# Performance work log

Hardware: AMD Instinct MI355X
Metric: run time of the kernel (lower is better)

## Reference

```python
import jax, jax.numpy as jnp
import numpy as np

VOCAB = 50257
BATCH = 512
SEQ = 1024


def setup_inputs() -> dict:
    key = jax.random.key(0)
    kx, kidf = jax.random.split(key)
    x = jax.random.randint(kx, (BATCH, SEQ), 0, VOCAB, dtype=jnp.int64)
    # idf weights are positive; uniform in (0.1, 5.0) mimics real idf values
    idf = jax.random.uniform(kidf, (VOCAB,), dtype=jnp.float32, minval=0.1, maxval=5.0)
    return {"x": x, "idf": idf}


def reference(x, idf):
    B, S = x.shape
    V = idf.shape[0]
    # term-frequency histogram: scatter-add directly into (B, V) accumulator,
    # equivalent to the one-hot scatter_ + sum over seq in the original
    rows = jnp.arange(B, dtype=x.dtype)[:, None]           # (B, 1)
    tf = jnp.zeros((B, V), dtype=jnp.float32).at[rows, x].add(1.0)
    tfidf = tf * idf                                        # (B, V)
    n = jnp.sum(tfidf, axis=1, keepdims=True)               # (B, 1)
    return tfidf / n
```

## Files before the change

kernel.cpp:

```cpp
#include <hip/hip_runtime.h>


constexpr int VOCAB   = 50257;
constexpr int SEQ     = 1024;
constexpr int BATCH   = 512;
constexpr int BWORDS  = (VOCAB + 3) / 4;
constexpr int BWORDS4 = ((BWORDS + 3) / 4) * 4;
constexpr int NT      = 1024;
constexpr int NGROUP  = VOCAB >> 2;

struct __attribute__((packed)) f4p { float4 v; };

__global__ __launch_bounds__(NT)
void tfidf_kernel(const int* __restrict__ x,
                  const float* __restrict__ idf,
                  float* __restrict__ out) {
    __shared__ __align__(16) unsigned int cnt[BWORDS4];
    __shared__ float red[NT / 64];

    const int b   = blockIdx.x;
    const int tid = threadIdx.x;

    const int tok = x[(size_t)b * SEQ + tid];

    {
        uint4* z = (uint4*)cnt;
        const uint4 z4 = make_uint4(0u, 0u, 0u, 0u);
        for (int i = tid; i < BWORDS4 / 4; i += NT) z[i] = z4;
    }

    const float my_idf = idf[tok];
    __syncthreads();

    atomicAdd(&cnt[tok >> 2], 1u << ((tok & 3) * 8));

    float v = my_idf;
    #pragma unroll
    for (int off = 32; off > 0; off >>= 1) v += __shfl_down(v, off, 64);
    if ((tid & 63) == 0) red[tid >> 6] = v;
    __syncthreads();
    float nsum = 0.0f;
    #pragma unroll
    for (int w = 0; w < NT / 64; ++w) nsum += red[w];
    const float inv_n = 1.0f / nsum;

    float* __restrict__ orow = out + (size_t)b * VOCAB;
    const float4* __restrict__ idf4 = (const float4*)idf;
    f4p* __restrict__ o4 = (f4p*)orow;

    for (int c = tid; c < NGROUP; c += NT) {
        const unsigned int w = cnt[c];
        const float4 f = idf4[c];
        float4 r;
        r.x = (float)(w & 0xffu)          * f.x * inv_n;
        r.y = (float)((w >> 8)  & 0xffu)  * f.y * inv_n;
        r.z = (float)((w >> 16) & 0xffu)  * f.z * inv_n;
        r.w = (float)(w >> 24)            * f.w * inv_n;
        o4[c].v = r;
    }
    if (tid == 0) {
        orow[VOCAB - 1] =
            (float)(cnt[(VOCAB - 1) >> 2] & 0xffu) * idf[VOCAB - 1] * inv_n;
    }
}

extern "C" void kernel_launch(void* const* d_in, const int* in_sizes, int n_in,
                              void* d_out, int out_size, void* d_ws, size_t ws_size,
                              hipStream_t stream) {
    const int*   x   = (const int*)d_in[0];
    const float* idf = (const float*)d_in[1];
    float*       out = (float*)d_out;
    tfidf_kernel<<<dim3(BATCH), dim3(NT), 0, stream>>>(x, idf, out);
}
```

Measured before the change: 110.8 us.

## Replace shared histogram with zero-fill plus global float atomics per token

Removes the LDS byte-packed histogram and the dense compute pass over the vocabulary. Each row of the output is zero-filled, and after the idf sum is reduced every token atomically adds idf*inv_n into its output slot in global memory. This drops the idf reads and LDS work of the dense pass. In exchange it issues 1024 global float atomics per row, which depend on the zero stores being visible (enforced by a vmcnt wait and a barrier), and float atomic ordering changes rounding slightly.

```diff
diff --git a/kernel.cpp b/kernel.cpp
--- a/kernel.cpp
+++ b/kernel.cpp
@@ -1,13 +1,11 @@
 #include <hip/hip_runtime.h>
 
 
-constexpr int VOCAB   = 50257;
-constexpr int SEQ     = 1024;
-constexpr int BATCH   = 512;
-constexpr int BWORDS  = (VOCAB + 3) / 4;
-constexpr int BWORDS4 = ((BWORDS + 3) / 4) * 4;
-constexpr int NT      = 1024;
-constexpr int NGROUP  = VOCAB >> 2;
+constexpr int VOCAB = 50257;
+constexpr int SEQ   = 1024;
+constexpr int BATCH = 512;
+constexpr int NT    = 1024;
+constexpr int NQUAD = VOCAB >> 2;
 
 struct __attribute__((packed)) f4p { float4 v; };
 
@@ -15,7 +13,6 @@
 void tfidf_kernel(const int* __restrict__ x,
                   const float* __restrict__ idf,
                   float* __restrict__ out) {
-    __shared__ __align__(16) unsigned int cnt[BWORDS4];
     __shared__ float red[NT / 64];
 
     const int b   = blockIdx.x;
@@ -23,45 +20,27 @@
 
     const int tok = x[(size_t)b * SEQ + tid];
 
-    {
-        uint4* z = (uint4*)cnt;
-        const uint4 z4 = make_uint4(0u, 0u, 0u, 0u);
-        for (int i = tid; i < BWORDS4 / 4; i += NT) z[i] = z4;
-    }
+    float* __restrict__ orow = out + (size_t)b * VOCAB;
+    f4p* __restrict__ o4 = (f4p*)orow;
+    const float4 z4 = make_float4(0.0f, 0.0f, 0.0f, 0.0f);
+    for (int c = tid; c < NQUAD; c += NT) o4[c].v = z4;
+    if (tid == 0) orow[VOCAB - 1] = 0.0f;
 
     const float my_idf = idf[tok];
-    __syncthreads();
-
-    atomicAdd(&cnt[tok >> 2], 1u << ((tok & 3) * 8));
-
     float v = my_idf;
     #pragma unroll
     for (int off = 32; off > 0; off >>= 1) v += __shfl_down(v, off, 64);
     if ((tid & 63) == 0) red[tid >> 6] = v;
+
+    asm volatile("s_waitcnt vmcnt(0)" ::: "memory");
     __syncthreads();
+
     float nsum = 0.0f;
     #pragma unroll
     for (int w = 0; w < NT / 64; ++w) nsum += red[w];
     const float inv_n = 1.0f / nsum;
 
-    float* __restrict__ orow = out + (size_t)b * VOCAB;
-    const float4* __restrict__ idf4 = (const float4*)idf;
-    f4p* __restrict__ o4 = (f4p*)orow;
-
-    for (int c = tid; c < NGROUP; c += NT) {
-        const unsigned int w = cnt[c];
-        const float4 f = idf4[c];
-        float4 r;
-        r.x = (float)(w & 0xffu)          * f.x * inv_n;
-        r.y = (float)((w >> 8)  & 0xffu)  * f.y * inv_n;
-        r.z = (float)((w >> 16) & 0xffu)  * f.z * inv_n;
-        r.w = (float)(w >> 24)            * f.w * inv_n;
-        o4[c].v = r;
-    }
-    if (tid == 0) {
-        orow[VOCAB - 1] =
-            (float)(cnt[(VOCAB - 1) >> 2] & 0xffu) * idf[VOCAB - 1] * inv_n;
-    }
+    atomicAdd(&orow[tok], my_idf * inv_n);
 }
 
 extern "C" void kernel_launch(void* const* d_in, const int* in_sizes, int n_in,
```

Result: slower. 127.8 us (+15.4%).
